# Kernel optimization log

Hardware: AMD Instinct MI355X
Metric: run time of the kernel (lower is better)

## Reference

```python
import jax, jax.numpy as jnp
import numpy as np
from jax import lax

B, C, D, H, W = 2, 64, 20, 20, 20


def _conv3d(x, w, b, pad):
    # x: [B,C,D,H,W], w: [O,I,kd,kh,kw]
    y = lax.conv_general_dilated(
        x, w, window_strides=(1, 1, 1), padding=pad,
        dimension_numbers=('NCDHW', 'OIDHW', 'NCDHW'))
    return y + b[None, :, None, None, None]


def setup_inputs() -> dict:
    key = jax.random.key(0)
    ks = jax.random.split(key, 7)
    s = 1.0 / np.sqrt(C * 3)  # conv fan-in = C*1*3*1
    return {
        'x': jax.random.normal(ks[0], (B, C, D, H, W), jnp.float32),
        'q_w': jax.random.uniform(ks[1], (C, C, 1, 3, 1), jnp.float32, -s, s),
        'q_b': jax.random.uniform(ks[2], (C,), jnp.float32, -s, s),
        'k_w': jax.random.uniform(ks[3], (C, C, 3, 1, 1), jnp.float32, -s, s),
        'k_b': jax.random.uniform(ks[4], (C,), jnp.float32, -s, s),
        'v_w': jax.random.uniform(ks[5], (C, C, 1, 1, 3), jnp.float32, -s, s),
        'v_b': jax.random.uniform(ks[6], (C,), jnp.float32, -s, s),
    }


def reference(x, q_w, q_b, k_w, k_b, v_w, v_b):
    b, c, d, h, w = x.shape
    n = d * h * w
    q0 = _conv3d(x, q_w, q_b, ((0, 0), (1, 1), (0, 0))).reshape(b, c, n)
    k0 = _conv3d(x, k_w, k_b, ((1, 1), (0, 0), (0, 0))).reshape(b, c, n)
    v = _conv3d(x, v_w, v_b, ((0, 0), (0, 0), (1, 1))).reshape(b, c, n)
    # scores[b, i, j] = sum_c k0[b,c,i] * q0[b,c,j]  -> [B, N, N]
    scores = jnp.einsum('bci,bcj->bij', k0, q0)
    # torch Softmax(dim=1) on [B,N,N] normalizes over axis 1 (the i axis)
    attn = jax.nn.softmax(scores, axis=1)
    out = jnp.einsum('bcn,bnm->bcm', v, attn)  # v @ attn
    return out.reshape(b, c, d, h, w)
```

## Files before the change

kernel.cpp:

```cpp
#include <hip/hip_runtime.h>
#include <cstdint>
#include <cstddef>

typedef _Float16 half4_t  __attribute__((ext_vector_type(4)));
typedef _Float16 half8_t  __attribute__((ext_vector_type(8)));
typedef short    short4_t __attribute__((ext_vector_type(4)));
typedef unsigned short ushort4_t __attribute__((ext_vector_type(4)));
typedef float    f32x4_t  __attribute__((ext_vector_type(4)));

#define LOG2E 1.44269504088896340736f

__device__ __forceinline__ float bf2f(unsigned short u) {
    union { unsigned int u; float f; } x;
    x.u = ((unsigned int)u) << 16;
    return x.f;
}
__device__ __forceinline__ unsigned short f2bf(float f) {
    union { float f; unsigned int u; } x;
    x.f = f;
    unsigned int r = (x.u + 0x7FFFu + ((x.u >> 16) & 1u)) >> 16;
    return (unsigned short)r;
}
__device__ __forceinline__ unsigned short f2bf_fast(float f) {
    union { float f; unsigned int u; } x;
    x.f = f;
    return (unsigned short)((x.u + 0x8000u) >> 16);
}

__global__ __launch_bounds__(256) void prep_kernel(
    const void* __restrict__ x,
    const void* __restrict__ qw, const void* __restrict__ kw, const void* __restrict__ vw,
    const void* __restrict__ qb, const void* __restrict__ kb, const void* __restrict__ vb,
    int* __restrict__ flag, _Float16* __restrict__ w2, float* __restrict__ bb)
{
    __shared__ int cnt;
    if (threadIdx.x == 0) cnt = 0;
    __syncthreads();
    {
        unsigned int w = ((const unsigned int*)x)[threadIdx.x];
        int e = (w >> 7) & 0xFF;
        int hit = (e == 0) || (e >= 0x68 && e <= 0x88);
        atomicAdd(&cnt, hit);
    }
    __syncthreads();
    const int bf = (cnt >= 128) ? 1 : 0;
    if (blockIdx.x == 0 && threadIdx.x == 0) flag[0] = bf;

    int idx = blockIdx.x * 256 + threadIdx.x;
    if (idx < 36864) {
        int conv = idx / 12288;
        int r    = idx - conv * 12288;
        int tap  = r >> 12;
        int r2   = r & 4095;
        int co   = r2 >> 6;
        int ci   = r2 & 63;
        const void* w = (conv == 0) ? qw : (conv == 1) ? kw : vw;
        float t;
        if (bf) t = bf2f(((const unsigned short*)w)[co * 192 + ci * 3 + tap]);
        else    t = ((const float*)w)[co * 192 + ci * 3 + tap];
        if (conv == 0) t *= LOG2E;
        w2[idx] = (_Float16)t;
    }
    if (idx < 192) {
        int a = idx >> 6, co = idx & 63;
        const void* s = (a == 0) ? qb : (a == 1) ? kb : vb;
        float t = bf ? bf2f(((const unsigned short*)s)[co]) : ((const float*)s)[co];
        if (a == 0) t *= LOG2E;
        bb[idx] = t;
    }
}

__global__ __launch_bounds__(256) void xt_kernel(
    const void* __restrict__ x, const int* __restrict__ flag, _Float16* __restrict__ xT)
{
    __shared__ _Float16 tile[64][66];
    const int bf   = *flag;
    const int lane = threadIdx.x & 63;
    const int wv   = threadIdx.x >> 6;
    const int n0   = blockIdx.x * 64;
    const int b    = blockIdx.y;

    if (bf) {
        const unsigned short* xb = (const unsigned short*)x + (size_t)b * 512000 + n0 + lane;
#pragma unroll
        for (int i = 0; i < 16; ++i) {
            const int ci = wv * 16 + i;
            tile[ci][lane] = (_Float16)bf2f(xb[(size_t)ci * 8000]);
        }
    } else {
        const float* xb = (const float*)x + (size_t)b * 512000 + n0 + lane;
#pragma unroll
        for (int i = 0; i < 16; ++i) {
            const int ci = wv * 16 + i;
            tile[ci][lane] = (_Float16)xb[(size_t)ci * 8000];
        }
    }
    __syncthreads();
    _Float16* out = xT + ((size_t)b * 8000 + n0) * 64 + lane;
#pragma unroll
    for (int i = 0; i < 16; ++i) {
        const int r = wv * 16 + i;
        out[(size_t)r * 64] = tile[lane][r];
    }
}

__global__ __launch_bounds__(256, 2) void convg_kernel(
    const _Float16* __restrict__ xT, const _Float16* __restrict__ w2,
    const float* __restrict__ bb,
    _Float16* __restrict__ Qt, _Float16* __restrict__ Kt, unsigned short* __restrict__ Vt)
{
    const int tid = threadIdx.x;
    const int wv  = tid >> 6;
    const int L   = tid & 63;
    const int q4  = L >> 4;
    const int lm  = L & 15;
    const int W    = blockIdx.x * 4 + wv;
    const int conv = W % 3;
    const int u    = W / 3;
    const int b    = u / 250;
    const int n0   = (u - b * 250) * 32;

    half8_t wf[3][2][4];
    const _Float16* wbase = w2 + (size_t)conv * 12288;
#pragma unroll
    for (int tap = 0; tap < 3; ++tap)
#pragma unroll
        for (int kh = 0; kh < 2; ++kh)
#pragma unroll
            for (int cb = 0; cb < 4; ++cb)
                wf[tap][kh][cb] = *(const half8_t*)(
                    wbase + ((size_t)(tap * 64 + cb * 16 + lm)) * 64 + kh * 32 + q4 * 8);

    f32x4_t acc[2][4];
#pragma unroll
    for (int cb = 0; cb < 4; ++cb) {
        const float bi = bb[conv * 64 + cb * 16 + lm];
        const f32x4_t v = (f32x4_t){bi, bi, bi, bi};
        acc[0][cb] = v;
        acc[1][cb] = v;
    }

    const _Float16* xb = xT + (size_t)b * 512000;
    const half8_t z8 = {(_Float16)0, (_Float16)0, (_Float16)0, (_Float16)0,
                        (_Float16)0, (_Float16)0, (_Float16)0, (_Float16)0};

#pragma unroll
    for (int mt = 0; mt < 2; ++mt) {
        const int npos = n0 + mt * 16 + lm;
        int gm, gp, off;
        if (conv == 0)      { const int h = (npos / 20) % 20; gm = h > 0; gp = h < 19; off = 20; }
        else if (conv == 1) { const int d = npos / 400;       gm = d > 0; gp = d < 19; off = 400; }
        else                { const int w = npos % 20;        gm = w > 0; gp = w < 19; off = 1; }
        const int rm = gm ? npos - off : npos;
        const int rp = gp ? npos + off : npos;

#pragma unroll
        for (int kh = 0; kh < 2; ++kh) {
            const int ko = kh * 32 + q4 * 8;
            half8_t a0 = *(const half8_t*)(xb + (size_t)rm * 64 + ko);
            const half8_t a1 = *(const half8_t*)(xb + (size_t)npos * 64 + ko);
            half8_t a2 = *(const half8_t*)(xb + (size_t)rp * 64 + ko);
            a0 = gm ? a0 : z8;
            a2 = gp ? a2 : z8;
#pragma unroll
            for (int cb = 0; cb < 4; ++cb) {
                acc[mt][cb] = __builtin_amdgcn_mfma_f32_16x16x32_f16(a0, wf[0][kh][cb], acc[mt][cb], 0, 0, 0);
                acc[mt][cb] = __builtin_amdgcn_mfma_f32_16x16x32_f16(a1, wf[1][kh][cb], acc[mt][cb], 0, 0, 0);
                acc[mt][cb] = __builtin_amdgcn_mfma_f32_16x16x32_f16(a2, wf[2][kh][cb], acc[mt][cb], 0, 0, 0);
            }
        }
    }

    if (conv < 2) {
        _Float16* dst = (conv == 0) ? Qt : Kt;
#pragma unroll
        for (int mt = 0; mt < 2; ++mt)
#pragma unroll
            for (int cb = 0; cb < 4; ++cb)
#pragma unroll
                for (int reg = 0; reg < 4; ++reg) {
                    const int n = n0 + mt * 16 + q4 * 4 + reg;
                    dst[((size_t)b * 8000 + n) * 64 + cb * 16 + lm] = (_Float16)acc[mt][cb][reg];
                }
    } else {
#pragma unroll
        for (int mt = 0; mt < 2; ++mt)
#pragma unroll
            for (int cb = 0; cb < 4; ++cb) {
                ushort4_t vvv;
#pragma unroll
                for (int reg = 0; reg < 4; ++reg) vvv[reg] = f2bf(acc[mt][cb][reg]);
                *(ushort4_t*)(Vt + ((size_t)b * 64 + cb * 16 + lm) * 8000 + n0 + mt * 16 + q4 * 4) = vvv;
            }
    }
}

__global__ __launch_bounds__(256, 2) void attn_kernel(
    const _Float16* __restrict__ Qt, const _Float16* __restrict__ Kt,
    const unsigned short* __restrict__ Vt,
    _Float16* __restrict__ Oseg, float* __restrict__ Wseg)
{
    __shared__ __align__(16) _Float16       k_lds[2][4096];
    __shared__ __align__(16) unsigned short v_lds[2][4096];

    const int tid = threadIdx.x;
    const int wv  = tid >> 6;
    const int L   = tid & 63;
    const int q4  = L >> 4;
    const int lm  = L & 15;
    const int qt  = blockIdx.x;
    const int b   = blockIdx.y;
    const int sp  = blockIdx.z;
    const int NS  = gridDim.z;
    const int t0  = (125 * sp) / NS;
    const int t1  = (125 * (sp + 1)) / NS;
    const int unit = qt * 4 + wv;

    const _Float16* Qb = Qt + ((size_t)b * 8000 + (size_t)qt * 128 + wv * 32 + lm) * 64 + q4 * 8;
    half8_t bq00 = *(const half8_t*)(Qb);
    half8_t bq01 = *(const half8_t*)(Qb + 32);
    half8_t bq10 = *(const half8_t*)(Qb + 16 * 64);
    half8_t bq11 = *(const half8_t*)(Qb + 16 * 64 + 32);

    f32x4_t o[2][4];
    float l_acc[2] = {0.f, 0.f};
#pragma unroll
    for (int mt = 0; mt < 2; ++mt)
#pragma unroll
        for (int cb = 0; cb < 4; ++cb) o[mt][cb] = (f32x4_t){0.f, 0.f, 0.f, 0.f};

    const _Float16*       Kg = Kt + (size_t)b * 512000;
    const unsigned short* Vg = Vt + (size_t)b * 512000;
    const int r0  = tid >> 3;
    const int cc0 = tid & 7;
    const int swz_lo = r0 * 64 + ((cc0 ^ (r0 & 7)) * 8);
    const int swz_hi = (r0 + 32) * 64 + ((cc0 ^ (r0 & 7)) * 8);
    const _Float16*       Kr0 = Kg + (size_t)r0 * 64 + cc0 * 8;
    const _Float16*       Kr1 = Kg + (size_t)(r0 + 32) * 64 + cc0 * 8;
    const unsigned short* Vr0 = Vg + (size_t)r0 * 8000 + cc0 * 8;
    const unsigned short* Vr1 = Vg + (size_t)(r0 + 32) * 8000 + cc0 * 8;

    uint4 sk0, sk1, sv0, sv1;

    {
        const int n0 = t0 * 64;
        sk0 = *(const uint4*)(Kr0 + (size_t)n0 * 64);
        sk1 = *(const uint4*)(Kr1 + (size_t)n0 * 64);
        sv0 = *(const uint4*)(Vr0 + n0);
        sv1 = *(const uint4*)(Vr1 + n0);
        *(uint4*)(&k_lds[0][swz_lo]) = sk0;
        *(uint4*)(&k_lds[0][swz_hi]) = sk1;
        *(uint4*)(&v_lds[0][swz_lo]) = sv0;
        *(uint4*)(&v_lds[0][swz_hi]) = sv1;
        if (t0 + 1 < t1) {
            const int n1 = (t0 + 1) * 64;
            sk0 = *(const uint4*)(Kr0 + (size_t)n1 * 64);
            sk1 = *(const uint4*)(Kr1 + (size_t)n1 * 64);
            sv0 = *(const uint4*)(Vr0 + n1);
            sv1 = *(const uint4*)(Vr1 + n1);
        }
    }

    int p = 0;
    for (int kt = t0; kt < t1; ++kt) {
        __syncthreads();
        if (kt + 1 < t1) {
            *(uint4*)(&k_lds[p ^ 1][swz_lo]) = sk0;
            *(uint4*)(&k_lds[p ^ 1][swz_hi]) = sk1;
            *(uint4*)(&v_lds[p ^ 1][swz_lo]) = sv0;
            *(uint4*)(&v_lds[p ^ 1][swz_hi]) = sv1;
            if (kt + 2 < t1) {
                const int n2 = (kt + 2) * 64;
                sk0 = *(const uint4*)(Kr0 + (size_t)n2 * 64);
                sk1 = *(const uint4*)(Kr1 + (size_t)n2 * 64);
                sv0 = *(const uint4*)(Vr0 + n2);
                sv1 = *(const uint4*)(Vr1 + n2);
            }
        }

        short4_t pfr[2][4];
        float la0 = 0.f, la1 = 0.f;
#pragma unroll
        for (int ns = 0; ns < 4; ++ns) {
            const int n = ns * 16 + lm;
            const _Float16* krow = &k_lds[p][n * 64];
            const half8_t ak0 = *(const half8_t*)(krow + (((q4    ) ^ (n & 7)) * 8));
            const half8_t ak1 = *(const half8_t*)(krow + (((q4 + 4) ^ (n & 7)) * 8));
#pragma unroll
            for (int mt = 0; mt < 2; ++mt) {
                f32x4_t z = (f32x4_t){0.f, 0.f, 0.f, 0.f};
                z = __builtin_amdgcn_mfma_f32_16x16x32_f16(ak0, mt ? bq10 : bq00, z, 0, 0, 0);
                z = __builtin_amdgcn_mfma_f32_16x16x32_f16(ak1, mt ? bq11 : bq01, z, 0, 0, 0);
                short4_t pk;
#pragma unroll
                for (int reg = 0; reg < 4; ++reg) {
                    const float pv = exp2f(z[reg]);
                    if (mt == 0) la0 += pv; else la1 += pv;
                    pk[reg] = (short)f2bf_fast(pv);
                }
                pfr[mt][ns] = pk;
            }
        }
        l_acc[0] += la0;
        l_acc[1] += la1;

#pragma unroll
        for (int cb = 0; cb < 4; ++cb) {
            const int c = cb * 16 + lm;
            const unsigned short* vrow = &v_lds[p][c * 64];
            f32x4_t a0 = o[0][cb], a1 = o[1][cb];
#pragma unroll
            for (int ns = 0; ns < 4; ++ns) {
                const int cc = ns * 2 + (q4 >> 1);
                const short4_t av = *(const short4_t*)(vrow + ((cc ^ (c & 7)) * 8) + (q4 & 1) * 4);
                a0 = __builtin_amdgcn_mfma_f32_16x16x16bf16_1k(av, pfr[0][ns], a0, 0, 0, 0);
                a1 = __builtin_amdgcn_mfma_f32_16x16x16bf16_1k(av, pfr[1][ns], a1, 0, 0, 0);
            }
            o[0][cb] = a0;
            o[1][cb] = a1;
        }
        p ^= 1;
    }

    if (unit >= 250) return;

    float rinv[2], lg[2];
#pragma unroll
    for (int mt = 0; mt < 2; ++mt) {
        float l = l_acc[mt];
        l += __shfl_xor(l, 16);
        l += __shfl_xor(l, 32);
        rinv[mt] = 1.0f / l;
        lg[mt]   = __log2f(l);
    }

    const int seg = (b * 250 + unit) * NS + sp;
    _Float16* os = Oseg + (size_t)seg * 2048;
#pragma unroll
    for (int mt = 0; mt < 2; ++mt) {
#pragma unroll
        for (int cb = 0; cb < 4; ++cb) {
            half4_t e;
#pragma unroll
            for (int reg = 0; reg < 4; ++reg) e[reg] = (_Float16)(o[mt][cb][reg] * rinv[mt]);
            *(half4_t*)(os + (mt * 16 + lm) * 64 + cb * 16 + q4 * 4) = e;
        }
    }
    if (q4 == 0) {
#pragma unroll
        for (int mt = 0; mt < 2; ++mt)
            Wseg[(size_t)seg * 32 + mt * 16 + lm] = lg[mt];
    }
}

__global__ __launch_bounds__(256, 2) void combine_kernel(
    const _Float16* __restrict__ Oseg, const float* __restrict__ Wseg,
    const int* __restrict__ flag, void* __restrict__ outv, int NS)
{
    __shared__ float wls[8 * 32];
    __shared__ float cls[8 * 32];
    const int tid = threadIdx.x;
    const int qt = blockIdx.x, b = blockIdx.y;
    const int base = (b * 250 + qt) * NS;

    for (int i = tid; i < NS * 32; i += 256) wls[i] = Wseg[(size_t)base * 32 + i];
    __syncthreads();
    if (tid < 32) {
        const int r = tid;
        float wm = wls[r];
        for (int s2 = 1; s2 < NS; ++s2) wm = fmaxf(wm, wls[s2 * 32 + r]);
        float cs = 0.f;
        for (int s2 = 0; s2 < NS; ++s2) {
            float cc = exp2f(wls[s2 * 32 + r] - wm);
            cls[s2 * 32 + r] = cc;
            cs += cc;
        }
        const float inv = 1.f / cs;
        for (int s2 = 0; s2 < NS; ++s2) cls[s2 * 32 + r] *= inv;
    }
    __syncthreads();

    const int c = tid & 63, rg = tid >> 6;
    float acc[8];
#pragma unroll
    for (int i = 0; i < 8; ++i) acc[i] = 0.f;
    for (int s2 = 0; s2 < NS; ++s2) {
        const _Float16* src = Oseg + ((size_t)(base + s2)) * 2048 + rg * 8 * 64 + c;
        const float* cf = &cls[s2 * 32 + rg * 8];
#pragma unroll
        for (int i = 0; i < 8; ++i) acc[i] += (float)src[i * 64] * cf[i];
    }

    const size_t ob = ((size_t)b * 64 + c) * 8000 + qt * 32 + rg * 8;
    if (*flag) {
        uint4 u0;
        u0.x = f2bf(acc[0]) | ((unsigned)f2bf(acc[1]) << 16);
        u0.y = f2bf(acc[2]) | ((unsigned)f2bf(acc[3]) << 16);
        u0.z = f2bf(acc[4]) | ((unsigned)f2bf(acc[5]) << 16);
        u0.w = f2bf(acc[6]) | ((unsigned)f2bf(acc[7]) << 16);
        *(uint4*)((unsigned short*)outv + ob) = u0;
    } else {
        float* o32 = (float*)outv + ob;
        *(f32x4_t*)(o32)     = (f32x4_t){acc[0], acc[1], acc[2], acc[3]};
        *(f32x4_t*)(o32 + 4) = (f32x4_t){acc[4], acc[5], acc[6], acc[7]};
    }
}

extern "C" void kernel_launch(void* const* d_in, const int* in_sizes, int n_in,
                              void* d_out, int out_size, void* d_ws, size_t ws_size,
                              hipStream_t stream)
{
    (void)in_sizes; (void)n_in; (void)out_size;
    const void* x  = d_in[0];
    const void* qw = d_in[1];
    const void* qb = d_in[2];
    const void* kw = d_in[3];
    const void* kb = d_in[4];
    const void* vw = d_in[5];
    const void* vb = d_in[6];

    char* ws = (char*)d_ws;
    int*            flag = (int*)ws;
    float*          bb   = (float*)(ws + 256);
    _Float16*       w2   = (_Float16*)(ws + 1024);
    _Float16*       Qt   = (_Float16*)(ws + 74752);
    _Float16*       Kt   = (_Float16*)(ws + 2122752);
    unsigned short* Vt   = (unsigned short*)(ws + 4170752);
    _Float16*       xT   = (_Float16*)(ws + 6218752);

    const size_t need8 = 23114752;
    const int NS = (ws_size >= need8) ? 8 : 1;
    _Float16* Oseg = (_Float16*)(ws + 6218752);
    float*    Wseg = (float*)(ws + 6218752 + (size_t)2 * 250 * NS * 2048 * 2);

    prep_kernel<<<dim3(144), 256, 0, stream>>>(x, qw, kw, vw, qb, kb, vb, flag, w2, bb);
    xt_kernel<<<dim3(125, 2), 256, 0, stream>>>(x, flag, xT);
    convg_kernel<<<dim3(375), 256, 0, stream>>>(xT, w2, bb, Qt, Kt, Vt);
    attn_kernel<<<dim3(63, 2, NS), 256, 0, stream>>>(Qt, Kt, Vt, Oseg, Wseg);
    combine_kernel<<<dim3(250, 2), 256, 0, stream>>>(Oseg, Wseg, flag, d_out, NS);
}
```

Measured before the change: 155.2 us.

## Fuse transpose into prep, merge combine into attention via last-arriver counter

Merges the x-transpose kernel into the prep kernel by adding extra blocks, and removes the separate combine kernel. Each attention wave now bumps a per-unit atomic counter, and the last split to finish does the cross-split softmax merge and writes the output. The row-sum of probabilities is also moved from scalar adds plus shuffles onto an MFMA against a ones vector. The aim is to cut launch count and the overhead of the combine pass. The cost is threadfences, atomics, and a serialized tail done by one wave per unit.

```diff
diff --git a/kernel.cpp b/kernel.cpp
--- a/kernel.cpp
+++ b/kernel.cpp
@@ -31,76 +31,79 @@
     const void* __restrict__ x,
     const void* __restrict__ qw, const void* __restrict__ kw, const void* __restrict__ vw,
     const void* __restrict__ qb, const void* __restrict__ kb, const void* __restrict__ vb,
-    int* __restrict__ flag, _Float16* __restrict__ w2, float* __restrict__ bb)
+    int* __restrict__ flag, int* __restrict__ cnt,
+    _Float16* __restrict__ w2, float* __restrict__ bb, _Float16* __restrict__ xT)
 {
-    __shared__ int cnt;
-    if (threadIdx.x == 0) cnt = 0;
+    __shared__ int scnt;
+    __shared__ _Float16 tile[64][66];
+
+    if (threadIdx.x == 0) scnt = 0;
     __syncthreads();
     {
         unsigned int w = ((const unsigned int*)x)[threadIdx.x];
         int e = (w >> 7) & 0xFF;
         int hit = (e == 0) || (e >= 0x68 && e <= 0x88);
-        atomicAdd(&cnt, hit);
+        atomicAdd(&scnt, hit);
     }
     __syncthreads();
-    const int bf = (cnt >= 128) ? 1 : 0;
-    if (blockIdx.x == 0 && threadIdx.x == 0) flag[0] = bf;
-
-    int idx = blockIdx.x * 256 + threadIdx.x;
-    if (idx < 36864) {
-        int conv = idx / 12288;
-        int r    = idx - conv * 12288;
-        int tap  = r >> 12;
-        int r2   = r & 4095;
-        int co   = r2 >> 6;
-        int ci   = r2 & 63;
-        const void* w = (conv == 0) ? qw : (conv == 1) ? kw : vw;
-        float t;
-        if (bf) t = bf2f(((const unsigned short*)w)[co * 192 + ci * 3 + tap]);
-        else    t = ((const float*)w)[co * 192 + ci * 3 + tap];
-        if (conv == 0) t *= LOG2E;
-        w2[idx] = (_Float16)t;
-    }
-    if (idx < 192) {
-        int a = idx >> 6, co = idx & 63;
-        const void* s = (a == 0) ? qb : (a == 1) ? kb : vb;
-        float t = bf ? bf2f(((const unsigned short*)s)[co]) : ((const float*)s)[co];
-        if (a == 0) t *= LOG2E;
-        bb[idx] = t;
-    }
-}
-
-__global__ __launch_bounds__(256) void xt_kernel(
-    const void* __restrict__ x, const int* __restrict__ flag, _Float16* __restrict__ xT)
-{
-    __shared__ _Float16 tile[64][66];
-    const int bf   = *flag;
-    const int lane = threadIdx.x & 63;
-    const int wv   = threadIdx.x >> 6;
-    const int n0   = blockIdx.x * 64;
-    const int b    = blockIdx.y;
-
-    if (bf) {
-        const unsigned short* xb = (const unsigned short*)x + (size_t)b * 512000 + n0 + lane;
+    const int bf = (scnt >= 128) ? 1 : 0;
+
+    const int gid = blockIdx.x * 256 + threadIdx.x;
+    if (gid < 500) cnt[gid] = 0;
+    if (gid == 0) flag[0] = bf;
+
+    if (blockIdx.x < 144) {
+        int idx = gid;
+        if (idx < 36864) {
+            int conv = idx / 12288;
+            int r    = idx - conv * 12288;
+            int tap  = r >> 12;
+            int r2   = r & 4095;
+            int co   = r2 >> 6;
+            int ci   = r2 & 63;
+            const void* w = (conv == 0) ? qw : (conv == 1) ? kw : vw;
+            float t;
+            if (bf) t = bf2f(((const unsigned short*)w)[co * 192 + ci * 3 + tap]);
+            else    t = ((const float*)w)[co * 192 + ci * 3 + tap];
+            if (conv == 0) t *= LOG2E;
+            w2[idx] = (_Float16)t;
+        }
+        if (idx < 192) {
+            int a = idx >> 6, co = idx & 63;
+            const void* s = (a == 0) ? qb : (a == 1) ? kb : vb;
+            float t = bf ? bf2f(((const unsigned short*)s)[co]) : ((const float*)s)[co];
+            if (a == 0) t *= LOG2E;
+            bb[idx] = t;
+        }
+    } else {
+        const int bx   = blockIdx.x - 144;
+        const int b    = bx / 125;
+        const int n0   = (bx - b * 125) * 64;
+        const int lane = threadIdx.x & 63;
+        const int wv   = threadIdx.x >> 6;
+
+        if (bf) {
+            const unsigned short* xb = (const unsigned short*)x + (size_t)b * 512000 + n0 + lane;
+#pragma unroll
+            for (int i = 0; i < 16; ++i) {
+                const int ci = wv * 16 + i;
+                tile[ci][lane] = (_Float16)bf2f(xb[(size_t)ci * 8000]);
+            }
+        } else {
+            const float* xb = (const float*)x + (size_t)b * 512000 + n0 + lane;
+#pragma unroll
+            for (int i = 0; i < 16; ++i) {
+                const int ci = wv * 16 + i;
+                tile[ci][lane] = (_Float16)xb[(size_t)ci * 8000];
+            }
+        }
+        __syncthreads();
+        _Float16* out = xT + ((size_t)b * 8000 + n0) * 64 + lane;
 #pragma unroll
         for (int i = 0; i < 16; ++i) {
-            const int ci = wv * 16 + i;
-            tile[ci][lane] = (_Float16)bf2f(xb[(size_t)ci * 8000]);
-        }
-    } else {
-        const float* xb = (const float*)x + (size_t)b * 512000 + n0 + lane;
-#pragma unroll
-        for (int i = 0; i < 16; ++i) {
-            const int ci = wv * 16 + i;
-            tile[ci][lane] = (_Float16)xb[(size_t)ci * 8000];
-        }
-    }
-    __syncthreads();
-    _Float16* out = xT + ((size_t)b * 8000 + n0) * 64 + lane;
-#pragma unroll
-    for (int i = 0; i < 16; ++i) {
-        const int r = wv * 16 + i;
-        out[(size_t)r * 64] = tile[lane][r];
+            const int r = wv * 16 + i;
+            out[(size_t)r * 64] = tile[lane][r];
+        }
     }
 }
 
@@ -198,7 +201,8 @@
 __global__ __launch_bounds__(256, 2) void attn_kernel(
     const _Float16* __restrict__ Qt, const _Float16* __restrict__ Kt,
     const unsigned short* __restrict__ Vt,
-    _Float16* __restrict__ Oseg, float* __restrict__ Wseg)
+    _Float16* __restrict__ Oseg, float* __restrict__ Wseg,
+    const int* __restrict__ flag, int* __restrict__ cnt, void* __restrict__ outv)
 {
     __shared__ __align__(16) _Float16       k_lds[2][4096];
     __shared__ __align__(16) unsigned short v_lds[2][4096];
@@ -223,11 +227,14 @@
     half8_t bq11 = *(const half8_t*)(Qb + 16 * 64 + 32);
 
     f32x4_t o[2][4];
-    float l_acc[2] = {0.f, 0.f};
-#pragma unroll
-    for (int mt = 0; mt < 2; ++mt)
+    f32x4_t acc_l[2];
+#pragma unroll
+    for (int mt = 0; mt < 2; ++mt) {
+        acc_l[mt] = (f32x4_t){0.f, 0.f, 0.f, 0.f};
 #pragma unroll
         for (int cb = 0; cb < 4; ++cb) o[mt][cb] = (f32x4_t){0.f, 0.f, 0.f, 0.f};
+    }
+    const short4_t ones4 = {(short)0x3F80, (short)0x3F80, (short)0x3F80, (short)0x3F80};
 
     const _Float16*       Kg = Kt + (size_t)b * 512000;
     const unsigned short* Vg = Vt + (size_t)b * 512000;
@@ -279,7 +286,6 @@
         }
 
         short4_t pfr[2][4];
-        float la0 = 0.f, la1 = 0.f;
 #pragma unroll
         for (int ns = 0; ns < 4; ++ns) {
             const int n = ns * 16 + lm;
@@ -293,16 +299,17 @@
                 z = __builtin_amdgcn_mfma_f32_16x16x32_f16(ak1, mt ? bq11 : bq01, z, 0, 0, 0);
                 short4_t pk;
 #pragma unroll
-                for (int reg = 0; reg < 4; ++reg) {
-                    const float pv = exp2f(z[reg]);
-                    if (mt == 0) la0 += pv; else la1 += pv;
-                    pk[reg] = (short)f2bf_fast(pv);
-                }
+                for (int reg = 0; reg < 4; ++reg)
+                    pk[reg] = (short)f2bf_fast(exp2f(z[reg]));
                 pfr[mt][ns] = pk;
             }
         }
-        l_acc[0] += la0;
-        l_acc[1] += la1;
+
+#pragma unroll
+        for (int mt = 0; mt < 2; ++mt)
+#pragma unroll
+            for (int ns = 0; ns < 4; ++ns)
+                acc_l[mt] = __builtin_amdgcn_mfma_f32_16x16x16bf16_1k(ones4, pfr[mt][ns], acc_l[mt], 0, 0, 0);
 
 #pragma unroll
         for (int cb = 0; cb < 4; ++cb) {
@@ -327,14 +334,13 @@
     float rinv[2], lg[2];
 #pragma unroll
     for (int mt = 0; mt < 2; ++mt) {
-        float l = l_acc[mt];
-        l += __shfl_xor(l, 16);
-        l += __shfl_xor(l, 32);
+        const float l = acc_l[mt][0];
         rinv[mt] = 1.0f / l;
         lg[mt]   = __log2f(l);
     }
 
-    const int seg = (b * 250 + unit) * NS + sp;
+    const int uidx = b * 250 + unit;
+    const int seg = uidx * NS + sp;
     _Float16* os = Oseg + (size_t)seg * 2048;
 #pragma unroll
     for (int mt = 0; mt < 2; ++mt) {
@@ -351,58 +357,64 @@
         for (int mt = 0; mt < 2; ++mt)
             Wseg[(size_t)seg * 32 + mt * 16 + lm] = lg[mt];
     }
-}
-
-__global__ __launch_bounds__(256, 2) void combine_kernel(
-    const _Float16* __restrict__ Oseg, const float* __restrict__ Wseg,
-    const int* __restrict__ flag, void* __restrict__ outv, int NS)
-{
-    __shared__ float wls[8 * 32];
-    __shared__ float cls[8 * 32];
-    const int tid = threadIdx.x;
-    const int qt = blockIdx.x, b = blockIdx.y;
-    const int base = (b * 250 + qt) * NS;
-
-    for (int i = tid; i < NS * 32; i += 256) wls[i] = Wseg[(size_t)base * 32 + i];
-    __syncthreads();
-    if (tid < 32) {
-        const int r = tid;
-        float wm = wls[r];
-        for (int s2 = 1; s2 < NS; ++s2) wm = fmaxf(wm, wls[s2 * 32 + r]);
+
+    __threadfence();
+    int old = 0;
+    if (L == 0) old = atomicAdd(&cnt[uidx], 1);
+    old = __shfl(old, 0, 64);
+    if (old != NS - 1) return;
+    __threadfence();
+
+    const int base = uidx * NS;
+    const int r = L & 31;
+    float cls[8];
+    {
+        float wsv[8];
+        float wm = -3.0e38f;
+#pragma unroll
+        for (int s = 0; s < 8; ++s) {
+            wsv[s] = (s < NS) ? Wseg[(size_t)(base + s) * 32 + r] : -3.0e38f;
+            wm = fmaxf(wm, wsv[s]);
+        }
         float cs = 0.f;
-        for (int s2 = 0; s2 < NS; ++s2) {
-            float cc = exp2f(wls[s2 * 32 + r] - wm);
-            cls[s2 * 32 + r] = cc;
-            cs += cc;
+#pragma unroll
+        for (int s = 0; s < 8; ++s) {
+            cls[s] = (s < NS) ? exp2f(wsv[s] - wm) : 0.f;
+            cs += cls[s];
         }
         const float inv = 1.f / cs;
-        for (int s2 = 0; s2 < NS; ++s2) cls[s2 * 32 + r] *= inv;
-    }
-    __syncthreads();
-
-    const int c = tid & 63, rg = tid >> 6;
-    float acc[8];
-#pragma unroll
-    for (int i = 0; i < 8; ++i) acc[i] = 0.f;
-    for (int s2 = 0; s2 < NS; ++s2) {
-        const _Float16* src = Oseg + ((size_t)(base + s2)) * 2048 + rg * 8 * 64 + c;
-        const float* cf = &cls[s2 * 32 + rg * 8];
-#pragma unroll
-        for (int i = 0; i < 8; ++i) acc[i] += (float)src[i * 64] * cf[i];
-    }
-
-    const size_t ob = ((size_t)b * 64 + c) * 8000 + qt * 32 + rg * 8;
-    if (*flag) {
-        uint4 u0;
-        u0.x = f2bf(acc[0]) | ((unsigned)f2bf(acc[1]) << 16);
-        u0.y = f2bf(acc[2]) | ((unsigned)f2bf(acc[3]) << 16);
-        u0.z = f2bf(acc[4]) | ((unsigned)f2bf(acc[5]) << 16);
-        u0.w = f2bf(acc[6]) | ((unsigned)f2bf(acc[7]) << 16);
-        *(uint4*)((unsigned short*)outv + ob) = u0;
-    } else {
-        float* o32 = (float*)outv + ob;
-        *(f32x4_t*)(o32)     = (f32x4_t){acc[0], acc[1], acc[2], acc[3]};
-        *(f32x4_t*)(o32 + 4) = (f32x4_t){acc[4], acc[5], acc[6], acc[7]};
+#pragma unroll
+        for (int s = 0; s < 8; ++s) cls[s] *= inv;
+    }
+
+    const int c = L;
+    const int bfv = *flag;
+#pragma unroll
+    for (int rc = 0; rc < 4; ++rc) {
+        float acc[8];
+#pragma unroll
+        for (int i = 0; i < 8; ++i) acc[i] = 0.f;
+#pragma unroll
+        for (int s = 0; s < 8; ++s) {
+            if (s < NS) {
+                const _Float16* src = Oseg + (size_t)(base + s) * 2048 + rc * 512 + c;
+#pragma unroll
+                for (int i = 0; i < 8; ++i) {
+                    const float w = __shfl(cls[s], rc * 8 + i, 64);
+                    acc[i] = fmaf((float)src[(size_t)i * 64], w, acc[i]);
+                }
+            }
+        }
+        const size_t ob = ((size_t)b * 64 + c) * 8000 + (size_t)unit * 32 + rc * 8;
+        if (bfv) {
+            unsigned short* o16 = (unsigned short*)outv + ob;
+#pragma unroll
+            for (int i = 0; i < 8; ++i) o16[i] = f2bf(acc[i]);
+        } else {
+            float* o32 = (float*)outv + ob;
+#pragma unroll
+            for (int i = 0; i < 8; ++i) o32[i] = acc[i];
+        }
     }
 }
 
@@ -421,21 +433,20 @@
 
     char* ws = (char*)d_ws;
     int*            flag = (int*)ws;
-    float*          bb   = (float*)(ws + 256);
-    _Float16*       w2   = (_Float16*)(ws + 1024);
-    _Float16*       Qt   = (_Float16*)(ws + 74752);
-    _Float16*       Kt   = (_Float16*)(ws + 2122752);
-    unsigned short* Vt   = (unsigned short*)(ws + 4170752);
-    _Float16*       xT   = (_Float16*)(ws + 6218752);
-
-    const size_t need8 = 23114752;
+    int*            cnt  = (int*)(ws + 256);
+    float*          bb   = (float*)(ws + 2304);
+    _Float16*       w2   = (_Float16*)(ws + 3072);
+    _Float16*       Qt   = (_Float16*)(ws + 76800);
+    _Float16*       Kt   = (_Float16*)(ws + 2124800);
+    unsigned short* Vt   = (unsigned short*)(ws + 4172800);
+    _Float16*       xT   = (_Float16*)(ws + 6220800);
+
+    const size_t need8 = 23116800;
     const int NS = (ws_size >= need8) ? 8 : 1;
-    _Float16* Oseg = (_Float16*)(ws + 6218752);
-    float*    Wseg = (float*)(ws + 6218752 + (size_t)2 * 250 * NS * 2048 * 2);
-
-    prep_kernel<<<dim3(144), 256, 0, stream>>>(x, qw, kw, vw, qb, kb, vb, flag, w2, bb);
-    xt_kernel<<<dim3(125, 2), 256, 0, stream>>>(x, flag, xT);
+    _Float16* Oseg = (_Float16*)(ws + 6220800);
+    float*    Wseg = (float*)(ws + 6220800 + (size_t)2 * 250 * NS * 2048 * 2);
+
+    prep_kernel<<<dim3(394), 256, 0, stream>>>(x, qw, kw, vw, qb, kb, vb, flag, cnt, w2, bb, xT);
     convg_kernel<<<dim3(375), 256, 0, stream>>>(xT, w2, bb, Qt, Kt, Vt);
-    attn_kernel<<<dim3(63, 2, NS), 256, 0, stream>>>(Qt, Kt, Vt, Oseg, Wseg);
-    combine_kernel<<<dim3(250, 2), 256, 0, stream>>>(Oseg, Wseg, flag, d_out, NS);
-}
+    attn_kernel<<<dim3(63, 2, NS), 256, 0, stream>>>(Qt, Kt, Vt, Oseg, Wseg, flag, cnt, d_out);
+}
```

New measurement: 284.5 us. 1.83x slower.
